# Performance work log

Hardware: AMD Instinct MI355X
Metric: run time of the kernel (lower is better)

Reference implementation:

```python
import jax, jax.numpy as jnp
import numpy as np

DIM = 2048; KV_RANK = 512; Q_RANK = 768; H = 16
D_NR = 128; D_R = 64; D_V = 128
B = 8; L = 32; MAX_T = 4096; START = MAX_T - L
QK_DIM = D_NR + D_R
SCALE = 1.0 / float(np.sqrt(QK_DIM))
EPS = 1.1920929e-07  # torch.finfo(float32).eps (nn.RMSNorm default)
ROPE_BASE = 10000.0


def rms_norm(x, w):
    return x * jax.lax.rsqrt(jnp.mean(x * x, axis=-1, keepdims=True) + EPS) * w


def apply_rope(x, cos, sin):
    # x: (b, l, h, d) with d even; cos/sin: (l, d//2) -> complex multiply on pairs
    b, l, h, d = x.shape
    xp = x.reshape(b, l, h, d // 2, 2)
    xr, xi = xp[..., 0], xp[..., 1]
    c = cos[None, :, None, :]
    s = sin[None, :, None, :]
    return jnp.stack([xr * c - xi * s, xr * s + xi * c], axis=-1).reshape(b, l, h, d)


def setup_inputs() -> dict:
    key = jax.random.key(0)
    ks = jax.random.split(key, 9)
    w = 0.02
    # rotary angles for absolute positions START..START+L-1
    inv_freq = 1.0 / (ROPE_BASE ** (np.arange(0, D_R, 2, dtype=np.float32) / D_R))  # (32,)
    pos = np.arange(START, START + L, dtype=np.float32)
    ang = pos[:, None] * inv_freq[None, :]  # (L, 32)
    # causal mask over full cache: query i sits at absolute position START+i
    t = jnp.arange(MAX_T)[None, :]
    qpos = START + jnp.arange(L)[:, None]
    mask = jnp.where(t <= qpos, 0.0, -1e30).astype(jnp.float32)  # (L, MAX_T)
    return {
        "x": jax.random.normal(ks[0], (B, L, DIM), dtype=jnp.float32),
        "start_pos": START,
        "freq_cos": jnp.asarray(np.cos(ang), dtype=jnp.float32),
        "freq_sin": jnp.asarray(np.sin(ang), dtype=jnp.float32),
        "mask": mask,
        "kv_latent_cache": jax.random.normal(ks[1], (B, MAX_T, KV_RANK), dtype=jnp.float32) * 0.05,
        "k_rope_cache": jax.random.normal(ks[2], (B, MAX_T, D_R), dtype=jnp.float32) * 0.05,
        "w_kv_down": jax.random.normal(ks[3], (KV_RANK + D_R, DIM), dtype=jnp.float32) * w,
        "w_q_down": jax.random.normal(ks[4], (Q_RANK, DIM), dtype=jnp.float32) * w,
        "rms_q_w": jnp.ones((Q_RANK,), dtype=jnp.float32),
        "w_q_up": jax.random.normal(ks[5], (H * QK_DIM, Q_RANK), dtype=jnp.float32) * w,
        "w_kv_up": jax.random.normal(ks[6], (H * (D_NR + D_V), KV_RANK), dtype=jnp.float32) * w,
        "w_out": jax.random.normal(ks[7], (DIM, H * D_V), dtype=jnp.float32) * w,
    }


def reference(x, start_pos, freq_cos, freq_sin, mask, kv_latent_cache, k_rope_cache,
              w_kv_down, w_q_down, rms_q_w, w_q_up, w_kv_up, w_out):
    b, l, _ = x.shape
    end_pos = start_pos + l
    # query path: down-proj -> RMSNorm -> up-proj (NOTE: module's rms_norm_kv is unused)
    q = rms_norm(x @ w_q_down.T, rms_q_w) @ w_q_up.T
    q = q.reshape(b, l, H, QK_DIM)
    q_nrope, q_rope = q[..., :D_NR], q[..., D_NR:]
    q_rope = apply_rope(q_rope, freq_cos, freq_sin)
    # latent kv path
    kv = x @ w_kv_down.T  # (b, l, KV_RANK + D_R)
    kv_latent, k_rope = kv[..., :KV_RANK], kv[..., KV_RANK:]
    k_rope = apply_rope(k_rope[:, :, None, :], freq_cos, freq_sin)[:, :, 0, :]
    # scatter-write into caches, then read prefix [:end_pos]
    kvc = kv_latent_cache.at[:, start_pos:end_pos].set(kv_latent)[:, :end_pos]  # (b, t, k)
    krc = k_rope_cache.at[:, start_pos:end_pos].set(k_rope)[:, :end_pos]        # (b, t, r)
    # weight absorption
    w_up = w_kv_up.reshape(H, D_NR + D_V, KV_RANK)
    q_abs = jnp.einsum('blhd,hdk->blhk', q_nrope, w_up[:, :D_NR])
    scores = (jnp.einsum('blhk,btk->blht', q_abs, kvc)
              + jnp.einsum('blhr,btr->blht', q_rope, krc)) * SCALE
    scores = scores + mask[None, :, None, :]
    p = jax.nn.softmax(scores, axis=-1)
    o = jnp.einsum('blht,btk->blhk', p, kvc)
    o = jnp.einsum('blhk,hdk->blhd', o, w_up[:, D_NR:])
    return o.reshape(b, l, H * D_V) @ w_out.T
```

## Files before the change

kernel.cpp:

```cpp
#include <hip/hip_runtime.h>
#include <math.h>

#define DIMX 2048
#define KV_RANK 512
#define Q_RANK 768
#define NH 16
#define D_NR 128
#define D_R 64
#define D_V 128
#define NB 8
#define NL 32
#define MAX_T 4096
#define STARTP (MAX_T - NL)
#define QK_DIM (D_NR + D_R)
#define ATT_SCALE 0.07216878364870323f
#define RMS_EPS 1.1920929e-07f

typedef unsigned short u16;
typedef __attribute__((ext_vector_type(4))) unsigned short u16x4;
typedef __attribute__((ext_vector_type(8))) unsigned short u16x8;
typedef __attribute__((ext_vector_type(8))) short short8;
typedef __attribute__((ext_vector_type(4))) float f32x4;

#define GLOBAL_AS __attribute__((address_space(1)))
#define LDS_AS __attribute__((address_space(3)))

#define NDOWN 1344
#define DPART ((long long)256 * NDOWN)

__device__ inline u16 f2b(float f) {
    union { float f; unsigned u; } v; v.f = f;
    unsigned r = (v.u + 0x7fffu + ((v.u >> 16) & 1u)) >> 16;
    return (u16)r;
}
__device__ inline float b2f(u16 u) {
    union { unsigned u; float f; } v; v.u = ((unsigned)u) << 16; return v.f;
}

template<int BM, int BN, int OUTMODE, bool GSWZ>
__global__ __launch_bounds__(256) void gemm_mfma(
    const u16* __restrict__ A, const u16* __restrict__ B, void* __restrict__ Cv,
    float* __restrict__ rs,
    int K, int lda, int ldb, int ldc,
    long long sA1, long long sA2, long long sB1, long long sB2,
    long long sC1, long long sC2, int nb2)
{
    constexpr int MFR = BM / 32;
    constexpr int NFR = BN / 32;
    int bx = blockIdx.x, by = blockIdx.y, bz = blockIdx.z;
    if (GSWZ) {
        int flat = bx + gridDim.x * (by + gridDim.y * bz);
        int nwg = gridDim.x * gridDim.y * gridDim.z;
        int lf = (flat & 7) * (nwg >> 3) + (flat >> 3);
        bx = lf % gridDim.x;
        int r = lf / gridDim.x;
        by = r % gridDim.y;
        bz = r / gridDim.y;
    }
    const int z1 = bz / nb2, z2 = bz % nb2;
    A += z1 * sA1 + z2 * sA2;
    B += z1 * sB1 + z2 * sB2;

    const int m0 = by * BM;
    const int n0 = bx * BN;
    const int tid = threadIdx.x;
    const int lane = tid & 63;
    const int wid = tid >> 6;
    const int wm = wid >> 1, wn = wid & 1;
    const int l15 = lane & 15;
    const int l4  = lane >> 4;

    __shared__ __align__(16) u16 As[2][BM * 32];
    __shared__ __align__(16) u16 Bs[2][BN * 32];

    constexpr int nA = BM / 16;
    constexpr int nB = BN / 16;

    auto stage = [&](int buf, int k0) {
        #pragma unroll
        for (int j = 0; j < nA / 4 + 1; ++j) {
            int jj = wid + j * 4;
            if (jj < nA) {
                int c = jj * 64 + lane;
                int row = c >> 2;
                int ksg = (c & 3) ^ ((row >> 1) & 3);
                const u16* src = A + (long long)(m0 + row) * lda + k0 + ksg * 8;
                __builtin_amdgcn_global_load_lds((const GLOBAL_AS void*)src,
                                                 (LDS_AS void*)&As[buf][jj * 512], 16, 0, 0);
            }
        }
        #pragma unroll
        for (int j = 0; j < nB / 4 + 1; ++j) {
            int jj = wid + j * 4;
            if (jj < nB) {
                int c = jj * 64 + lane;
                int row = c >> 2;
                int ksg = (c & 3) ^ ((row >> 1) & 3);
                const u16* src = B + (long long)(n0 + row) * ldb + k0 + ksg * 8;
                __builtin_amdgcn_global_load_lds((const GLOBAL_AS void*)src,
                                                 (LDS_AS void*)&Bs[buf][jj * 512], 16, 0, 0);
            }
        }
    };

    f32x4 acc[MFR][NFR];
    #pragma unroll
    for (int i = 0; i < MFR; ++i)
        #pragma unroll
        for (int j = 0; j < NFR; ++j)
            acc[i][j] = (f32x4)0.0f;

    const int nk = K >> 5;
    stage(0, 0);
    int cur = 0;
    for (int ki = 0; ki < nk; ++ki) {
        __syncthreads();
        if (ki + 1 < nk) stage(cur ^ 1, (ki + 1) << 5);

        short8 a[MFR], b[NFR];
        #pragma unroll
        for (int mf = 0; mf < MFR; ++mf) {
            int row = wm * 16 * MFR + mf * 16 + l15;
            int ksl = l4 ^ ((row >> 1) & 3);
            a[mf] = *(const short8*)&As[cur][row * 32 + ksl * 8];
        }
        #pragma unroll
        for (int nf = 0; nf < NFR; ++nf) {
            int row = wn * 16 * NFR + nf * 16 + l15;
            int ksl = l4 ^ ((row >> 1) & 3);
            b[nf] = *(const short8*)&Bs[cur][row * 32 + ksl * 8];
        }
        __builtin_amdgcn_s_setprio(1);
        #pragma unroll
        for (int mf = 0; mf < MFR; ++mf)
            #pragma unroll
            for (int nf = 0; nf < NFR; ++nf)
                acc[mf][nf] = __builtin_amdgcn_mfma_f32_16x16x32_bf16(
                    a[mf], b[nf], acc[mf][nf], 0, 0, 0);
        __builtin_amdgcn_s_setprio(0);
        cur ^= 1;
    }

    if (OUTMODE == 2) {
        u16* C = (u16*)Cv + z1 * sC1 + z2 * sC2;
        float rowp[MFR][4];
        #pragma unroll
        for (int mf = 0; mf < MFR; ++mf)
            #pragma unroll
            for (int r = 0; r < 4; ++r)
                rowp[mf][r] = 0.f;
        #pragma unroll
        for (int mf = 0; mf < MFR; ++mf) {
            #pragma unroll
            for (int nf = 0; nf < NFR; ++nf) {
                int r0 = m0 + wm * 16 * MFR + mf * 16 + l4 * 4;
                int c0 = n0 + wn * 16 * NFR + nf * 16 + l15;
                #pragma unroll
                for (int r = 0; r < 4; ++r) {
                    int row = r0 + r;
                    int vlen = STARTP + (row & 31) + 1;
                    float p = (c0 < vlen) ? __expf(acc[mf][nf][r] * ATT_SCALE) : 0.f;
                    u16 pb = f2b(p);
                    C[(long long)row * ldc + c0] = pb;
                    rowp[mf][r] += b2f(pb);
                }
            }
        }
        #pragma unroll
        for (int mf = 0; mf < MFR; ++mf)
            #pragma unroll
            for (int r = 0; r < 4; ++r) {
                float v = rowp[mf][r];
                v += __shfl_xor(v, 1);
                v += __shfl_xor(v, 2);
                v += __shfl_xor(v, 4);
                v += __shfl_xor(v, 8);
                if (l15 == 0) {
                    int row = m0 + wm * 16 * MFR + mf * 16 + l4 * 4 + r;
                    atomicAdd(&rs[z1 * 512 + row], v);
                }
            }
    } else if (OUTMODE == 1) {
        u16* C = (u16*)Cv + z1 * sC1 + z2 * sC2;
        #pragma unroll
        for (int mf = 0; mf < MFR; ++mf)
            #pragma unroll
            for (int nf = 0; nf < NFR; ++nf) {
                int r0 = m0 + wm * 16 * MFR + mf * 16 + l4 * 4;
                int c0 = n0 + wn * 16 * NFR + nf * 16 + l15;
                #pragma unroll
                for (int r = 0; r < 4; ++r)
                    C[(long long)(r0 + r) * ldc + c0] = f2b(acc[mf][nf][r]);
            }
    } else {
        float* C = (float*)Cv + z1 * sC1 + z2 * sC2;
        #pragma unroll
        for (int mf = 0; mf < MFR; ++mf)
            #pragma unroll
            for (int nf = 0; nf < NFR; ++nf) {
                int r0 = m0 + wm * 16 * MFR + mf * 16 + l4 * 4;
                int c0 = n0 + wn * 16 * NFR + nf * 16 + l15;
                #pragma unroll
                for (int r = 0; r < 4; ++r)
                    C[(long long)(r0 + r) * ldc + c0] = acc[mf][nf][r];
            }
    }
}

struct Segs {
    const float* src[6];
    u16* dst[6];
    int n4[6];
};
__global__ __launch_bounds__(256) void f2b_multi(Segs s)
{
    int seg = blockIdx.y;
    int i = blockIdx.x * 256 + threadIdx.x;
    if (i >= s.n4[seg]) return;
    float4 v = ((const float4*)s.src[seg])[i];
    u16x4 o = { f2b(v.x), f2b(v.y), f2b(v.z), f2b(v.w) };
    ((u16x4*)s.dst[seg])[i] = o;
}

__global__ __launch_bounds__(256) void rs_zero(float* __restrict__ rs)
{
    int i = blockIdx.x * 256 + threadIdx.x;
    float4 z = { 0.f, 0.f, 0.f, 0.f };
    ((float4*)rs)[i] = z;
}

__global__ __launch_bounds__(256) void rms_reduce(const float* __restrict__ part,
                                                  const float* __restrict__ w,
                                                  u16* __restrict__ outb)
{
    const int row = blockIdx.x;
    const int tid = threadIdx.x;
    __shared__ float red[256];
    float val[3];
    float s = 0.f;
    #pragma unroll
    for (int j = 0; j < 3; ++j) {
        int i = tid + j * 256;
        long long off = (long long)row * NDOWN + i;
        float v = part[off] + part[DPART + off] + part[2 * DPART + off] + part[3 * DPART + off];
        val[j] = v;
        s += v * v;
    }
    red[tid] = s; __syncthreads();
    for (int off = 128; off > 0; off >>= 1) {
        if (tid < off) red[tid] += red[tid + off];
        __syncthreads();
    }
    float scale = rsqrtf(red[0] / (float)Q_RANK + RMS_EPS);
    u16* ob = outb + (long long)row * Q_RANK;
    #pragma unroll
    for (int j = 0; j < 3; ++j) {
        int i = tid + j * 256;
        ob[i] = f2b(val[j] * scale * w[i]);
    }
}

__global__ __launch_bounds__(256) void wuT_kernel(const float* __restrict__ w,
                                                  u16* __restrict__ outp)
{
    __shared__ u16 T[64][65];
    const int h = blockIdx.z;
    const int y0 = blockIdx.y * 64;
    const int x0 = blockIdx.x * 64;
    const int tid = threadIdx.x;
    #pragma unroll
    for (int i = 0; i < 16; ++i) {
        int lin = i * 256 + tid;
        int r = lin >> 6, c = lin & 63;
        T[c][r] = f2b(w[((long long)h * 256 + y0 + r) * 512 + x0 + c]);
    }
    __syncthreads();
    #pragma unroll
    for (int i = 0; i < 16; ++i) {
        int lin = i * 256 + tid;
        int r = lin >> 6, c = lin & 63;
        outp[((long long)h * 512 + x0 + r) * 128 + y0 + c] = T[r][c];
    }
}

__global__ __launch_bounds__(256) void bcat_new_reduce(const float* __restrict__ part,
                                                       const float* __restrict__ fc,
                                                       const float* __restrict__ fs,
                                                       u16* __restrict__ bcat)
{
    const int bl = blockIdx.x;
    const int b = bl >> 5, l = bl & 31;
    const int t = threadIdx.x;
    if (t >= 144) return;
    long long off = (long long)bl * NDOWN + 768 + 4 * t;
    float4 v0 = *(const float4*)(part + off);
    float4 v1 = *(const float4*)(part + DPART + off);
    float4 v2 = *(const float4*)(part + 2 * DPART + off);
    float4 v3 = *(const float4*)(part + 3 * DPART + off);
    float4 v = { v0.x + v1.x + v2.x + v3.x, v0.y + v1.y + v2.y + v3.y,
                 v0.z + v1.z + v2.z + v3.z, v0.w + v1.w + v2.w + v3.w };
    u16* dst = bcat + ((long long)b * MAX_T + STARTP + l) * 576;
    if (t < 128) {
        u16x4 o = { f2b(v.x), f2b(v.y), f2b(v.z), f2b(v.w) };
        ((u16x4*)dst)[t] = o;
    } else {
        int g = t - 128;
        float c0 = fc[l * 32 + 2 * g],     s0 = fs[l * 32 + 2 * g];
        float c1 = fc[l * 32 + 2 * g + 1], s1 = fs[l * 32 + 2 * g + 1];
        u16x4 o = { f2b(v.x * c0 - v.y * s0), f2b(v.x * s0 + v.y * c0),
                    f2b(v.z * c1 - v.w * s1), f2b(v.z * s1 + v.w * c1) };
        *(u16x4*)(dst + 512 + 4 * g) = o;
    }
}

__global__ __launch_bounds__(256) void prep_cache(const float* __restrict__ kvc,
                                                  const float* __restrict__ krc,
                                                  u16* __restrict__ bcat,
                                                  u16* __restrict__ kvcT)
{
    const int b = blockIdx.z;
    const int t0 = blockIdx.y * 64;
    const int tid = threadIdx.x;

    if (blockIdx.x == 8) {
        #pragma unroll
        for (int i = 0; i < 2; ++i) {
            int lin = i * 256 + tid;
            int r = lin >> 3, c8 = lin & 7;
            int t = t0 + r;
            if (t >= STARTP) continue;
            const float* src = krc + ((long long)b * MAX_T + t) * D_R + 8 * c8;
            float4 v0 = *(const float4*)src;
            float4 v1 = *(const float4*)(src + 4);
            u16x8 o = { f2b(v0.x), f2b(v0.y), f2b(v0.z), f2b(v0.w),
                        f2b(v1.x), f2b(v1.y), f2b(v1.z), f2b(v1.w) };
            *(u16x8*)(bcat + ((long long)b * MAX_T + t) * 576 + 512 + 8 * c8) = o;
        }
        return;
    }

    __shared__ u16 T[64 * 64];
    const int k0 = blockIdx.x * 64;

    #pragma unroll
    for (int i = 0; i < 2; ++i) {
        int lin = i * 256 + tid;
        int r = lin >> 3, c8 = lin & 7;
        int t = t0 + r;
        u16x4 oa, ob;
        if (t < STARTP) {
            const float* src = kvc + ((long long)b * MAX_T + t) * KV_RANK + k0 + 8 * c8;
            float4 v0 = *(const float4*)src;
            float4 v1 = *(const float4*)(src + 4);
            oa[0] = f2b(v0.x); oa[1] = f2b(v0.y); oa[2] = f2b(v0.z); oa[3] = f2b(v0.w);
            ob[0] = f2b(v1.x); ob[1] = f2b(v1.y); ob[2] = f2b(v1.z); ob[3] = f2b(v1.w);
            u16x8 o = { oa[0], oa[1], oa[2], oa[3], ob[0], ob[1], ob[2], ob[3] };
            *(u16x8*)(bcat + ((long long)b * MAX_T + t) * 576 + k0 + 8 * c8) = o;
        } else {
            const u16* s = bcat + ((long long)b * MAX_T + t) * 576 + k0 + 8 * c8;
            oa = *(const u16x4*)s;
            ob = *(const u16x4*)(s + 4);
        }
        int tg = r >> 2, te = r & 3;
        int c4a = 2 * c8, c4b = 2 * c8 + 1;
        int cola = ((tg ^ c4a) << 2) + te;
        int colb = ((tg ^ c4b) << 2) + te;
        #pragma unroll
        for (int j = 0; j < 4; ++j) {
            T[(4 * c4a + j) * 64 + cola] = oa[j];
            T[(4 * c4b + j) * 64 + colb] = ob[j];
        }
    }
    __syncthreads();

    u16* outp = kvcT + ((long long)b * KV_RANK + k0) * MAX_T + t0;
    #pragma unroll
    for (int i = 0; i < 2; ++i) {
        int lin = i * 256 + tid;
        int k = lin >> 3, c8 = lin & 7;
        int s = k >> 2;
        u16x4 va = *(const u16x4*)&T[k * 64 + (((2 * c8) ^ s) << 2)];
        u16x4 vb = *(const u16x4*)&T[k * 64 + (((2 * c8 + 1) ^ s) << 2)];
        u16x8 o = { va[0], va[1], va[2], va[3], vb[0], vb[1], vb[2], vb[3] };
        *(u16x8*)(outp + (long long)k * MAX_T + 8 * c8) = o;
    }
}

__global__ __launch_bounds__(256) void rope_q(const u16* __restrict__ qb,
                                              const float* __restrict__ fc,
                                              const float* __restrict__ fs,
                                              u16* __restrict__ qprimeb)
{
    int idx = blockIdx.x * 256 + threadIdx.x;
    int i = idx & 31;
    int h = (idx >> 5) & (NH - 1);
    int l = (idx >> 9) & (NL - 1);
    int b = idx >> 14;
    const u16* src = qb + (long long)(b * NL + l) * 3072 + h * QK_DIM + D_NR + 2 * i;
    float xr = b2f(src[0]), xi = b2f(src[1]);
    float c = fc[l * 32 + i], s = fs[l * 32 + i];
    u16* dst = qprimeb + ((long long)(b * NH + h) * NL + l) * 576 + 512 + 2 * i;
    dst[0] = f2b(xr * c - xi * s);
    dst[1] = f2b(xr * s + xi * c);
}

__global__ __launch_bounds__(256) void reduce_pv(const float* __restrict__ part,
                                                 const float* __restrict__ rs,
                                                 u16* __restrict__ o_hb)
{
    int idx = blockIdx.x * 256 + threadIdx.x;
    int b = idx >> 16;
    int i4 = idx & 65535;
    int m = i4 >> 7;
    const float* p = part + (long long)b * 1048576 + 4 * i4;
    float4 v0 = *(const float4*)p;
    float4 v1 = *(const float4*)(p + 262144);
    float4 v2 = *(const float4*)(p + 524288);
    float4 v3 = *(const float4*)(p + 786432);
    float inv = 1.0f / rs[b * 512 + m];
    u16x4 o = { f2b((v0.x + v1.x + v2.x + v3.x) * inv),
                f2b((v0.y + v1.y + v2.y + v3.y) * inv),
                f2b((v0.z + v1.z + v2.z + v3.z) * inv),
                f2b((v0.w + v1.w + v2.w + v3.w) * inv) };
    ((u16x4*)(o_hb + (long long)b * 262144))[i4] = o;
}

__global__ __launch_bounds__(256) void reduce_out(const float* __restrict__ part,
                                                  float* __restrict__ out)
{
    int idx = blockIdx.x * 256 + threadIdx.x;
    const float* p = part + 4 * (long long)idx;
    float4 v0 = *(const float4*)p;
    float4 v1 = *(const float4*)(p + 524288);
    float4 v2 = *(const float4*)(p + 1048576);
    float4 v3 = *(const float4*)(p + 1572864);
    float4 o = { v0.x + v1.x + v2.x + v3.x, v0.y + v1.y + v2.y + v3.y,
                 v0.z + v1.z + v2.z + v3.z, v0.w + v1.w + v2.w + v3.w };
    ((float4*)out)[idx] = o;
}

extern "C" void kernel_launch(void* const* d_in, const int* in_sizes, int n_in,
                              void* d_out, int out_size, void* d_ws, size_t ws_size,
                              hipStream_t stream)
{
    const float* x        = (const float*)d_in[0];
    const float* fc       = (const float*)d_in[2];
    const float* fs       = (const float*)d_in[3];
    const float* kvc      = (const float*)d_in[5];
    const float* krc      = (const float*)d_in[6];
    const float* w_kv_down= (const float*)d_in[7];
    const float* w_q_down = (const float*)d_in[8];
    const float* rms_q_w  = (const float*)d_in[9];
    const float* w_q_up   = (const float*)d_in[10];
    const float* w_kv_up  = (const float*)d_in[11];
    const float* w_out    = (const float*)d_in[12];
    float* out            = (float*)d_out;

    float* down_part = (float*)d_ws;
    float* rs      = down_part + 1376256;
    u16* pb        = (u16*)(rs + 4096);
    u16* base      = pb + 16777216;
    u16* xb      = base;                 base += 524288;
    u16* qdb     = base;                 base += 196608;
    u16* qb      = base;                 base += 786432;
    u16* qprimeb = base;                 base += 2359296;
    u16* wqkv_b  = base;                 base += 2752512;
    u16* wqu_b   = base;                 base += 2359296;
    u16* wkvu_b  = base;                 base += 2097152;
    u16* wout_b  = base;                 base += 4194304;
    u16* wuT     = base;                 base += 1048576;
    u16* bcat    = base;                 base += 18874368;
    u16* kvcT    = base;                 base += 16777216;
    u16* o_hb    = base;                 base += 2097152;
    u16* o_upb   = base;                 base += 524288;
    float* pv_part  = (float*)bcat;
    float* out_part = (float*)kvcT;

    Segs segs;
    segs.src[0] = x;         segs.dst[0] = xb;                  segs.n4[0] = 131072;
    segs.src[1] = w_q_down;  segs.dst[1] = wqkv_b;              segs.n4[1] = 393216;
    segs.src[2] = w_q_up;    segs.dst[2] = wqu_b;               segs.n4[2] = 589824;
    segs.src[3] = w_kv_down; segs.dst[3] = wqkv_b + 768 * 2048; segs.n4[3] = 294912;
    segs.src[4] = w_kv_up;   segs.dst[4] = wkvu_b;              segs.n4[4] = 524288;
    segs.src[5] = w_out;     segs.dst[5] = wout_b;              segs.n4[5] = 1048576;
    f2b_multi<<<dim3(4096, 6), 256, 0, stream>>>(segs);

    rs_zero<<<4, 256, 0, stream>>>(rs);
    wuT_kernel<<<dim3(8, 2, 16), 256, 0, stream>>>(w_kv_up, wuT);

    gemm_mfma<32, 64, 0, true><<<dim3(21, 8, 4), 256, 0, stream>>>(
        xb, wqkv_b, down_part, nullptr, 512, 2048, 2048, NDOWN,
        0LL, 512LL, 0LL, 512LL, 0LL, DPART, 4);
    rms_reduce<<<256, 256, 0, stream>>>(down_part, rms_q_w, qdb);
    gemm_mfma<32, 64, 1, true><<<dim3(48, 8, 1), 256, 0, stream>>>(
        qdb, wqu_b, qb, nullptr, 768, 768, 768, 3072, 0, 0, 0, 0, 0, 0, 1);
    bcat_new_reduce<<<256, 256, 0, stream>>>(down_part, fc, fs, bcat);
    prep_cache<<<dim3(9, 64, 8), 256, 0, stream>>>(kvc, krc, bcat, kvcT);

    gemm_mfma<32, 128, 1, true><<<dim3(4, 1, 128), 256, 0, stream>>>(
        qb, wuT, qprimeb, nullptr, 128, 3072, 128, 576,
        98304LL, 192LL, 0LL, 65536LL, 294912LL, 18432LL, 16);
    rope_q<<<512, 256, 0, stream>>>(qb, fc, fs, qprimeb);

    gemm_mfma<128, 128, 2, true><<<dim3(32, 4, 8), 256, 0, stream>>>(
        qprimeb, bcat, pb, rs, 576, 576, 576, 4096,
        294912LL, 0LL, 2359296LL, 0LL, 2097152LL, 0LL, 1);
    gemm_mfma<128, 128, 0, true><<<dim3(4, 4, 32), 256, 0, stream>>>(
        pb, kvcT, pv_part, nullptr, 1024, 4096, 4096, 512,
        2097152LL, 1024LL, 2097152LL, 1024LL, 1048576LL, 262144LL, 4);
    reduce_pv<<<2048, 256, 0, stream>>>(pv_part, rs, o_hb);

    gemm_mfma<32, 64, 1, true><<<dim3(2, 1, 128), 256, 0, stream>>>(
        o_hb, wkvu_b + 128 * 512, o_upb, nullptr, 512, 512, 512, 2048,
        262144LL, 16384LL, 0LL, 131072LL, 65536LL, 128LL, 16);
    gemm_mfma<32, 64, 0, true><<<dim3(32, 8, 4), 256, 0, stream>>>(
        o_upb, wout_b, out_part, nullptr, 512, 2048, 2048, 2048,
        0LL, 512LL, 0LL, 512LL, 0LL, 524288LL, 4);
    reduce_out<<<512, 256, 0, stream>>>(out_part, out);
}
```

Baseline: 317.3 us.

## Fuse QK scores, exp and PV into one flash-style attention kernel

Replaces the separate score GEMM (which wrote the exponentiated probabilities P as a bf16 matrix of 16M elements) and the PV GEMM with a single kernel. Each block holds a 32-row query tile in LDS, streams K tiles in with async global-to-LDS loads, computes exp scores into a small LDS P tile and immediately multiplies by V read directly from global memory. Row sums are written per time-split partial instead of using atomics, which removes the rs_zero kernel. The grid shrinks to 512 blocks and V is loaded without LDS staging, so occupancy and V load efficiency could limit it.

Measured after the change: 361.3 us. 13.9% more time.

```diff
diff --git a/kernel.cpp b/kernel.cpp
--- a/kernel.cpp
+++ b/kernel.cpp
@@ -37,10 +37,9 @@
     union { unsigned u; float f; } v; v.u = ((unsigned)u) << 16; return v.f;
 }
 
-template<int BM, int BN, int OUTMODE, bool GSWZ>
+template<int BM, int BN, bool OUTB, bool GSWZ>
 __global__ __launch_bounds__(256) void gemm_mfma(
     const u16* __restrict__ A, const u16* __restrict__ B, void* __restrict__ Cv,
-    float* __restrict__ rs,
     int K, int lda, int ldb, int ldc,
     long long sA1, long long sA2, long long sB1, long long sB2,
     long long sC1, long long sC2, int nb2)
@@ -141,46 +140,7 @@
         cur ^= 1;
     }
 
-    if (OUTMODE == 2) {
-        u16* C = (u16*)Cv + z1 * sC1 + z2 * sC2;
-        float rowp[MFR][4];
-        #pragma unroll
-        for (int mf = 0; mf < MFR; ++mf)
-            #pragma unroll
-            for (int r = 0; r < 4; ++r)
-                rowp[mf][r] = 0.f;
-        #pragma unroll
-        for (int mf = 0; mf < MFR; ++mf) {
-            #pragma unroll
-            for (int nf = 0; nf < NFR; ++nf) {
-                int r0 = m0 + wm * 16 * MFR + mf * 16 + l4 * 4;
-                int c0 = n0 + wn * 16 * NFR + nf * 16 + l15;
-                #pragma unroll
-                for (int r = 0; r < 4; ++r) {
-                    int row = r0 + r;
-                    int vlen = STARTP + (row & 31) + 1;
-                    float p = (c0 < vlen) ? __expf(acc[mf][nf][r] * ATT_SCALE) : 0.f;
-                    u16 pb = f2b(p);
-                    C[(long long)row * ldc + c0] = pb;
-                    rowp[mf][r] += b2f(pb);
-                }
-            }
-        }
-        #pragma unroll
-        for (int mf = 0; mf < MFR; ++mf)
-            #pragma unroll
-            for (int r = 0; r < 4; ++r) {
-                float v = rowp[mf][r];
-                v += __shfl_xor(v, 1);
-                v += __shfl_xor(v, 2);
-                v += __shfl_xor(v, 4);
-                v += __shfl_xor(v, 8);
-                if (l15 == 0) {
-                    int row = m0 + wm * 16 * MFR + mf * 16 + l4 * 4 + r;
-                    atomicAdd(&rs[z1 * 512 + row], v);
-                }
-            }
-    } else if (OUTMODE == 1) {
+    if (OUTB) {
         u16* C = (u16*)Cv + z1 * sC1 + z2 * sC2;
         #pragma unroll
         for (int mf = 0; mf < MFR; ++mf)
@@ -207,6 +167,165 @@
     }
 }
 
+__global__ __launch_bounds__(256) void attn_fused(
+    const u16* __restrict__ qp,
+    const u16* __restrict__ bcat,
+    const u16* __restrict__ kvcT,
+    float* __restrict__ opart,
+    float* __restrict__ rspart)
+{
+    int flat = blockIdx.x + gridDim.x * (blockIdx.y + gridDim.y * blockIdx.z);
+    int lf = (flat & 7) * 64 + (flat >> 3);
+    const int mb = lf & 15;
+    const int ts = (lf >> 4) & 3;
+    const int b  = lf >> 6;
+    const int m0 = mb * 32;
+
+    const int tid = threadIdx.x;
+    const int lane = tid & 63;
+    const int w = tid >> 6;
+    const int l15 = lane & 15;
+    const int l4  = lane >> 4;
+
+    __shared__ __align__(16) u16 Qs[32 * 584];
+    __shared__ __align__(16) u16 Ks[2][128 * 64];
+    __shared__ __align__(16) u16 Ps[32 * 128];
+    __shared__ float rs_l[4][32];
+
+    const u16* qsrc = qp + ((long long)b * 512 + m0) * 576;
+    #pragma unroll
+    for (int i = 0; i < 9; ++i) {
+        int idx = i * 256 + tid;
+        int row = idx / 72, c8 = idx % 72;
+        *(u16x8*)&Qs[row * 584 + c8 * 8] = *(const u16x8*)&qsrc[(long long)row * 576 + c8 * 8];
+    }
+
+    const int tb0 = ts * 1024;
+    const u16* Kbase = bcat + (long long)b * MAX_T * 576;
+    const u16* Vbase = kvcT + (long long)b * 512 * 4096;
+
+    auto stageK = [&](int buf, int tile, int k0) {
+        #pragma unroll
+        for (int j = 0; j < 4; ++j) {
+            int c = (w * 4 + j) * 64 + lane;
+            int row = c >> 3;
+            int g = (c & 7) ^ (row & 7);
+            const u16* src = Kbase + (long long)(tb0 + tile * 128 + row) * 576 + k0 + g * 8;
+            __builtin_amdgcn_global_load_lds((const GLOBAL_AS void*)src,
+                                             (LDS_AS void*)&Ks[buf][c * 8], 16, 0, 0);
+        }
+    };
+
+    f32x4 acc[2][8];
+    #pragma unroll
+    for (int i = 0; i < 2; ++i)
+        #pragma unroll
+        for (int j = 0; j < 8; ++j)
+            acc[i][j] = (f32x4)0.0f;
+    float rsum[2][4];
+    #pragma unroll
+    for (int i = 0; i < 2; ++i)
+        #pragma unroll
+        for (int r = 0; r < 4; ++r)
+            rsum[i][r] = 0.f;
+
+    stageK(0, 0, 0);
+    int cur = 0;
+    for (int tile = 0; tile < 8; ++tile) {
+        f32x4 sacc[2][2];
+        #pragma unroll
+        for (int i = 0; i < 2; ++i)
+            #pragma unroll
+            for (int j = 0; j < 2; ++j)
+                sacc[i][j] = (f32x4)0.0f;
+
+        for (int kc = 0; kc < 9; ++kc) {
+            __syncthreads();
+            if (kc < 8) stageK(cur ^ 1, tile, (kc + 1) * 64);
+            else if (tile < 7) stageK(cur ^ 1, tile + 1, 0);
+
+            __builtin_amdgcn_s_setprio(1);
+            #pragma unroll
+            for (int kk = 0; kk < 2; ++kk) {
+                int kg = kc * 64 + kk * 32;
+                short8 a0 = *(const short8*)&Qs[(l15) * 584 + kg + l4 * 8];
+                short8 a1 = *(const short8*)&Qs[(16 + l15) * 584 + kg + l4 * 8];
+                #pragma unroll
+                for (int tf = 0; tf < 2; ++tf) {
+                    int trow = w * 32 + tf * 16 + l15;
+                    int slot = (kk * 4 + l4) ^ (trow & 7);
+                    short8 bb = *(const short8*)&Ks[cur][trow * 64 + slot * 8];
+                    sacc[0][tf] = __builtin_amdgcn_mfma_f32_16x16x32_bf16(a0, bb, sacc[0][tf], 0, 0, 0);
+                    sacc[1][tf] = __builtin_amdgcn_mfma_f32_16x16x32_bf16(a1, bb, sacc[1][tf], 0, 0, 0);
+                }
+            }
+            __builtin_amdgcn_s_setprio(0);
+            cur ^= 1;
+        }
+
+        #pragma unroll
+        for (int mf = 0; mf < 2; ++mf)
+            #pragma unroll
+            for (int tf = 0; tf < 2; ++tf)
+                #pragma unroll
+                for (int r = 0; r < 4; ++r) {
+                    int m = mf * 16 + l4 * 4 + r;
+                    int tl = w * 32 + tf * 16 + l15;
+                    int tg = tb0 + tile * 128 + tl;
+                    float p = (tg <= STARTP + (m & 31)) ? __expf(sacc[mf][tf][r] * ATT_SCALE) : 0.f;
+                    u16 pb2 = f2b(p);
+                    rsum[mf][r] += b2f(pb2);
+                    int slot = (tl >> 3) ^ (m & 15);
+                    Ps[m * 128 + (slot << 3) + (tl & 7)] = pb2;
+                }
+        __syncthreads();
+
+        #pragma unroll
+        for (int tc = 0; tc < 4; ++tc) {
+            short8 a[2];
+            #pragma unroll
+            for (int mf = 0; mf < 2; ++mf) {
+                int m = mf * 16 + l15;
+                int slot = (tc * 4 + l4) ^ (m & 15);
+                a[mf] = *(const short8*)&Ps[m * 128 + (slot << 3)];
+            }
+            long long tg0 = tb0 + tile * 128 + tc * 32 + l4 * 8;
+            #pragma unroll
+            for (int nf = 0; nf < 8; ++nf) {
+                int n = w * 128 + nf * 16 + l15;
+                short8 bb = *(const short8*)&Vbase[(long long)n * 4096 + tg0];
+                acc[0][nf] = __builtin_amdgcn_mfma_f32_16x16x32_bf16(a[0], bb, acc[0][nf], 0, 0, 0);
+                acc[1][nf] = __builtin_amdgcn_mfma_f32_16x16x32_bf16(a[1], bb, acc[1][nf], 0, 0, 0);
+            }
+        }
+    }
+
+    float* od = opart + ((long long)b * 4 + ts) * 262144 + (long long)m0 * 512;
+    #pragma unroll
+    for (int mf = 0; mf < 2; ++mf)
+        #pragma unroll
+        for (int nf = 0; nf < 8; ++nf)
+            #pragma unroll
+            for (int r = 0; r < 4; ++r)
+                od[(long long)(mf * 16 + l4 * 4 + r) * 512 + w * 128 + nf * 16 + l15] = acc[mf][nf][r];
+
+    #pragma unroll
+    for (int mf = 0; mf < 2; ++mf)
+        #pragma unroll
+        for (int r = 0; r < 4; ++r) {
+            float v = rsum[mf][r];
+            v += __shfl_xor(v, 1);
+            v += __shfl_xor(v, 2);
+            v += __shfl_xor(v, 4);
+            v += __shfl_xor(v, 8);
+            if (l15 == 0) rs_l[w][mf * 16 + l4 * 4 + r] = v;
+        }
+    __syncthreads();
+    if (tid < 32)
+        rspart[((long long)ts * 8 + b) * 512 + m0 + tid] =
+            rs_l[0][tid] + rs_l[1][tid] + rs_l[2][tid] + rs_l[3][tid];
+}
+
 struct Segs {
     const float* src[6];
     u16* dst[6];
@@ -220,13 +339,6 @@
     float4 v = ((const float4*)s.src[seg])[i];
     u16x4 o = { f2b(v.x), f2b(v.y), f2b(v.z), f2b(v.w) };
     ((u16x4*)s.dst[seg])[i] = o;
-}
-
-__global__ __launch_bounds__(256) void rs_zero(float* __restrict__ rs)
-{
-    int i = blockIdx.x * 256 + threadIdx.x;
-    float4 z = { 0.f, 0.f, 0.f, 0.f };
-    ((float4*)rs)[i] = z;
 }
 
 __global__ __launch_bounds__(256) void rms_reduce(const float* __restrict__ part,
@@ -405,7 +517,7 @@
 }
 
 __global__ __launch_bounds__(256) void reduce_pv(const float* __restrict__ part,
-                                                 const float* __restrict__ rs,
+                                                 const float* __restrict__ rsp,
                                                  u16* __restrict__ o_hb)
 {
     int idx = blockIdx.x * 256 + threadIdx.x;
@@ -417,7 +529,9 @@
     float4 v1 = *(const float4*)(p + 262144);
     float4 v2 = *(const float4*)(p + 524288);
     float4 v3 = *(const float4*)(p + 786432);
-    float inv = 1.0f / rs[b * 512 + m];
+    float denom = rsp[b * 512 + m] + rsp[4096 + b * 512 + m]
+                + rsp[8192 + b * 512 + m] + rsp[12288 + b * 512 + m];
+    float inv = 1.0f / denom;
     u16x4 o = { f2b((v0.x + v1.x + v2.x + v3.x) * inv),
                 f2b((v0.y + v1.y + v2.y + v3.y) * inv),
                 f2b((v0.z + v1.z + v2.z + v3.z) * inv),
@@ -457,9 +571,9 @@
     float* out            = (float*)d_out;
 
     float* down_part = (float*)d_ws;
-    float* rs      = down_part + 1376256;
-    u16* pb        = (u16*)(rs + 4096);
-    u16* base      = pb + 16777216;
+    float* rs_part   = down_part;
+    float* pv_part   = down_part + 1376256;
+    u16* base      = (u16*)(pv_part + 8388608);
     u16* xb      = base;                 base += 524288;
     u16* qdb     = base;                 base += 196608;
     u16* qb      = base;                 base += 786432;
@@ -473,7 +587,6 @@
     u16* kvcT    = base;                 base += 16777216;
     u16* o_hb    = base;                 base += 2097152;
     u16* o_upb   = base;                 base += 524288;
-    float* pv_part  = (float*)bcat;
     float* out_part = (float*)kvcT;
 
     Segs segs;
@@ -485,36 +598,31 @@
     segs.src[5] = w_out;     segs.dst[5] = wout_b;              segs.n4[5] = 1048576;
     f2b_multi<<<dim3(4096, 6), 256, 0, stream>>>(segs);
 
-    rs_zero<<<4, 256, 0, stream>>>(rs);
     wuT_kernel<<<dim3(8, 2, 16), 256, 0, stream>>>(w_kv_up, wuT);
 
-    gemm_mfma<32, 64, 0, true><<<dim3(21, 8, 4), 256, 0, stream>>>(
-        xb, wqkv_b, down_part, nullptr, 512, 2048, 2048, NDOWN,
+    gemm_mfma<32, 64, false, true><<<dim3(21, 8, 4), 256, 0, stream>>>(
+        xb, wqkv_b, down_part, 512, 2048, 2048, NDOWN,
         0LL, 512LL, 0LL, 512LL, 0LL, DPART, 4);
     rms_reduce<<<256, 256, 0, stream>>>(down_part, rms_q_w, qdb);
-    gemm_mfma<32, 64, 1, true><<<dim3(48, 8, 1), 256, 0, stream>>>(
-        qdb, wqu_b, qb, nullptr, 768, 768, 768, 3072, 0, 0, 0, 0, 0, 0, 1);
+    gemm_mfma<32, 64, true, true><<<dim3(48, 8, 1), 256, 0, stream>>>(
+        qdb, wqu_b, qb, 768, 768, 768, 3072, 0, 0, 0, 0, 0, 0, 1);
     bcat_new_reduce<<<256, 256, 0, stream>>>(down_part, fc, fs, bcat);
     prep_cache<<<dim3(9, 64, 8), 256, 0, stream>>>(kvc, krc, bcat, kvcT);
 
-    gemm_mfma<32, 128, 1, true><<<dim3(4, 1, 128), 256, 0, stream>>>(
-        qb, wuT, qprimeb, nullptr, 128, 3072, 128, 576,
+    gemm_mfma<32, 128, true, true><<<dim3(4, 1, 128), 256, 0, stream>>>(
+        qb, wuT, qprimeb, 128, 3072, 128, 576,
         98304LL, 192LL, 0LL, 65536LL, 294912LL, 18432LL, 16);
     rope_q<<<512, 256, 0, stream>>>(qb, fc, fs, qprimeb);
 
-    gemm_mfma<128, 128, 2, true><<<dim3(32, 4, 8), 256, 0, stream>>>(
-        qprimeb, bcat, pb, rs, 576, 576, 576, 4096,
-        294912LL, 0LL, 2359296LL, 0LL, 2097152LL, 0LL, 1);
-    gemm_mfma<128, 128, 0, true><<<dim3(4, 4, 32), 256, 0, stream>>>(
-        pb, kvcT, pv_part, nullptr, 1024, 4096, 4096, 512,
-        2097152LL, 1024LL, 2097152LL, 1024LL, 1048576LL, 262144LL, 4);
-    reduce_pv<<<2048, 256, 0, stream>>>(pv_part, rs, o_hb);
-
-    gemm_mfma<32, 64, 1, true><<<dim3(2, 1, 128), 256, 0, stream>>>(
-        o_hb, wkvu_b + 128 * 512, o_upb, nullptr, 512, 512, 512, 2048,
+    attn_fused<<<dim3(16, 4, 8), 256, 0, stream>>>(
+        qprimeb, bcat, kvcT, pv_part, rs_part);
+    reduce_pv<<<2048, 256, 0, stream>>>(pv_part, rs_part, o_hb);
+
+    gemm_mfma<32, 64, true, true><<<dim3(2, 1, 128), 256, 0, stream>>>(
+        o_hb, wkvu_b + 128 * 512, o_upb, 512, 512, 512, 2048,
         262144LL, 16384LL, 0LL, 131072LL, 65536LL, 128LL, 16);
-    gemm_mfma<32, 64, 0, true><<<dim3(32, 8, 4), 256, 0, stream>>>(
-        o_upb, wout_b, out_part, nullptr, 512, 2048, 2048, 2048,
+    gemm_mfma<32, 64, false, true><<<dim3(32, 8, 4), 256, 0, stream>>>(
+        o_upb, wout_b, out_part, 512, 2048, 2048, 2048,
         0LL, 512LL, 0LL, 512LL, 0LL, 524288LL, 4);
     reduce_out<<<512, 256, 0, stream>>>(out_part, out);
 }
```
